# Kernel optimization log

Measured on AMD Instinct MI355X. Metric: run time of the kernel, lower is better.

## Reference

```python
import jax, jax.numpy as jnp
import numpy as np

N_NODES = 50000
N_EDGES = 800000
F_IN = 128
F_OUT = 64


def setup_inputs() -> dict:
    key = jax.random.key(0)
    k_x, k_w, k_r, k_c, k_v = jax.random.split(key, 5)
    x = jax.random.normal(k_x, (N_NODES, F_IN), dtype=jnp.float32)
    weight = jax.random.normal(k_w, (F_IN, F_OUT), dtype=jnp.float32)
    edge_row = jnp.sort(jax.random.randint(k_r, (N_EDGES,), 0, N_NODES, dtype=jnp.int32))
    edge_col = jax.random.randint(k_c, (N_EDGES,), 0, N_NODES, dtype=jnp.int32)
    edge_val = jax.random.uniform(k_v, (N_EDGES,), dtype=jnp.float32)
    return {"x": x, "weight": weight, "edge_row": edge_row,
            "edge_col": edge_col, "edge_val": edge_val}


def reference(x, weight, edge_row, edge_col, edge_val):
    # pre_sup = dot(x, W)                      : [N, F_out] dense GEMM
    pre_sup = x @ weight
    # support @ pre_sup (sparse-dense matmul) via COO gather + segment sum:
    # out[r] = sum_{e: row[e]==r} val[e] * pre_sup[col[e]]
    msgs = edge_val[:, None] * pre_sup[edge_col]          # [E, F_out]
    out = jax.ops.segment_sum(msgs, edge_row, num_segments=N_NODES)
    # act = relu, no bias
    return jax.nn.relu(out)
```

## Files before the change

kernel.cpp:

```cpp
#include <hip/hip_runtime.h>
#include <hip/hip_bf16.h>

#define F_IN 128
#define F_OUT 64

typedef __attribute__((ext_vector_type(8))) short short8;
typedef __attribute__((ext_vector_type(4))) float f32x4;

__device__ __forceinline__ unsigned short f2bf_rne(float f) {
  unsigned int u = __builtin_bit_cast(unsigned int, f);
  u += 0x7fffu + ((u >> 16) & 1u);
  return (unsigned short)(u >> 16);
}
__device__ __forceinline__ float bfu2f(unsigned short u) {
  return __builtin_bit_cast(float, (unsigned int)u << 16);
}

__global__ __launch_bounds__(256) void gcn_gemm_rowptr(
    const float* __restrict__ x, const float* __restrict__ w,
    unsigned short* __restrict__ pre,
    const int* __restrict__ edge_row, int* __restrict__ row_ptr,
    int n_nodes, int n_edges, int gemm_blocks) {
  const int tid = threadIdx.x;

  if (blockIdx.x >= gemm_blocks) {
    const int r = (blockIdx.x - gemm_blocks) * 256 + tid;
    if (r > n_nodes) return;
    int lo = 0, hi = n_edges;
    while (lo < hi) {
      const int mid = (lo + hi) >> 1;
      if (edge_row[mid] < r) lo = mid + 1; else hi = mid;
    }
    row_ptr[r] = lo;
    return;
  }

  __shared__ __align__(16) unsigned short wt_hi[64 * 128];

  {
#pragma unroll
    for (int i = 0; i < 8; ++i) {
      const int flat4 = tid + i * 256;
      const float4 v = ((const float4*)w)[flat4];
      const float fv[4] = {v.x, v.y, v.z, v.w};
#pragma unroll
      for (int j = 0; j < 4; ++j) {
        const int flat = flat4 * 4 + j;
        const int k = flat >> 6;
        const int n = flat & 63;
        int off = (n << 8) + (k << 1);
        off ^= (n & 7) << 4;
        *(unsigned short*)((char*)wt_hi + off) = f2bf_rne(fv[j]);
      }
    }
  }
  __syncthreads();

  const int lane = tid & 63;
  const int mt = blockIdx.x * 4 + (tid >> 6);
  const int m0 = mt * 16;
  if (m0 >= n_nodes) return;

  const int lrow = lane & 15;
  const int lk = lane >> 4;
  const bool full = (m0 + 16 <= n_nodes);
  const int arow = full ? (m0 + lrow) : min(m0 + lrow, n_nodes - 1);

  f32x4 acc[4];
#pragma unroll
  for (int i = 0; i < 4; ++i) acc[i] = (f32x4){0.f, 0.f, 0.f, 0.f};

#pragma unroll
  for (int ks = 0; ks < 4; ++ks) {
    const float4* xp =
        (const float4*)(x + (size_t)arow * F_IN + ks * 32 + lk * 8);
    const float4 q0 = xp[0];
    const float4 q1 = xp[1];
    const float fv[8] = {q0.x, q0.y, q0.z, q0.w, q1.x, q1.y, q1.z, q1.w};
    short8 ah, al;
#pragma unroll
    for (int i = 0; i < 8; ++i) {
      const unsigned short h = f2bf_rne(fv[i]);
      ah[i] = (short)h;
      al[i] = (short)f2bf_rne(fv[i] - bfu2f(h));
    }
#pragma unroll
    for (int nt = 0; nt < 4; ++nt) {
      const int n = nt * 16 + lrow;
      int off = (n << 8) + (ks * 64 + lk * 16);
      off ^= (n & 7) << 4;
      const short8 bh = *(const short8*)((const char*)wt_hi + off);
      acc[nt] = __builtin_amdgcn_mfma_f32_16x16x32_bf16(ah, bh, acc[nt], 0, 0, 0);
      acc[nt] = __builtin_amdgcn_mfma_f32_16x16x32_bf16(al, bh, acc[nt], 0, 0, 0);
    }
  }

#pragma unroll
  for (int nt = 0; nt < 4; ++nt) {
#pragma unroll
    for (int r = 0; r < 4; ++r) {
      const int row = m0 + lk * 4 + r;
      if (full || row < n_nodes)
        pre[(size_t)row * F_OUT + nt * 16 + lrow] = f2bf_rne(acc[nt][r]);
    }
  }
}

__global__ __launch_bounds__(256) void gcn_spmm(
    const unsigned short* __restrict__ pre, const int* __restrict__ row_ptr,
    const int* __restrict__ edge_col, const float* __restrict__ edge_val,
    float* __restrict__ out, int n_nodes) {
  const int lane = threadIdx.x & 63;
  const int half = lane >> 5;
  const int fl = lane & 31;
  int row = (int)((blockIdx.x * blockDim.x + threadIdx.x) >> 6);
  row = __builtin_amdgcn_readfirstlane(row);
  if (row >= n_nodes) return;
  const int e0 = row_ptr[row];
  const int e1 = row_ptr[row + 1];

  float a0 = 0.f, a1 = 0.f, a2 = 0.f, a3 = 0.f;

  for (int base = e0; base < e1; base += 64) {
    const int cnt = min(64, e1 - base);
    int myc = 0;
    float myv = 0.f;
    if (lane < cnt) {
      myc = edge_col[base + lane] << 6;
      myv = edge_val[base + lane];
    }
    const int nb = (cnt + 15) >> 4;
    for (int b = 0; b < nb; ++b) {
      const int j0 = b * 16;
#pragma unroll
      for (int u = 0; u < 8; u += 2) {
        const int i0 = j0 + u * 2 + half;
        const int i1 = j0 + (u + 1) * 2 + half;
        const int c0 = __shfl(myc, i0);
        const float v0 = __shfl(myv, i0);
        const int c1 = __shfl(myc, i1);
        const float v1 = __shfl(myv, i1);
        const unsigned int p0 =
            *(const unsigned int*)((const char*)pre + ((size_t)c0 << 1) + (fl << 2));
        const unsigned int p1 =
            *(const unsigned int*)((const char*)pre + ((size_t)c1 << 1) + (fl << 2));
        a0 = fmaf(v0, bfu2f((unsigned short)(p0 & 0xffff)), a0);
        a1 = fmaf(v0, bfu2f((unsigned short)(p0 >> 16)), a1);
        a2 = fmaf(v1, bfu2f((unsigned short)(p1 & 0xffff)), a2);
        a3 = fmaf(v1, bfu2f((unsigned short)(p1 >> 16)), a3);
      }
    }
  }

  float s0 = (a0 + a2) + __shfl_xor(a0 + a2, 32);
  float s1 = (a1 + a3) + __shfl_xor(a1 + a3, 32);
  if (half == 0) {
    float2 o = make_float2(fmaxf(s0, 0.f), fmaxf(s1, 0.f));
    *(float2*)(out + (size_t)row * F_OUT + fl * 2) = o;
  }
}

extern "C" void kernel_launch(void* const* d_in, const int* in_sizes, int n_in,
                              void* d_out, int out_size, void* d_ws, size_t ws_size,
                              hipStream_t stream) {
  const float* x        = (const float*)d_in[0];
  const float* w        = (const float*)d_in[1];
  const int*   edge_row = (const int*)d_in[2];
  const int*   edge_col = (const int*)d_in[3];
  const float* edge_val = (const float*)d_in[4];
  float* out = (float*)d_out;

  const int n_nodes = in_sizes[0] / F_IN;
  const int n_edges = in_sizes[2];

  unsigned short* pre = (unsigned short*)d_ws;
  int* row_ptr = (int*)((char*)d_ws +
                        (size_t)n_nodes * F_OUT * sizeof(unsigned short));

  const int m_tiles = (n_nodes + 15) / 16;
  const int gemm_blocks = (m_tiles + 3) / 4;
  const int rp_blocks = (n_nodes + 1 + 255) / 256;
  gcn_gemm_rowptr<<<gemm_blocks + rp_blocks, 256, 0, stream>>>(
      x, w, pre, edge_row, row_ptr, n_nodes, n_edges, gemm_blocks);

  const int spmm_blocks = ((size_t)n_nodes * 64 + 255) / 256;
  gcn_spmm<<<spmm_blocks, 256, 0, stream>>>(pre, row_ptr, edge_col, edge_val,
                                            out, n_nodes);
}
```

Baseline: 32.65 us.

## Split SpMM wave into four edge groups with 8-byte gathers

Restructures the SpMM so each wavefront processes four edges at once, with 16 lanes per edge each loading 4 bf16 features (uint2) instead of two edges with 32 lanes loading 2 features. Edge indices and values are read directly with uniform scalar loads instead of being staged into lanes and broadcast via shuffles, and a tail loop handles leftovers. Partial sums are reduced with two xor-shuffle stages before a float4 write of the relu'd output. This is meant to cut shuffle overhead and widen the gather loads, at the cost of a deeper cross-lane reduction and more per-iteration scalar loads.

```diff
diff --git a/kernel.cpp b/kernel.cpp
--- a/kernel.cpp
+++ b/kernel.cpp
@@ -14,6 +14,12 @@
 }
 __device__ __forceinline__ float bfu2f(unsigned short u) {
   return __builtin_bit_cast(float, (unsigned int)u << 16);
+}
+__device__ __forceinline__ float bf_lo(unsigned int u) {
+  return __builtin_bit_cast(float, u << 16);
+}
+__device__ __forceinline__ float bf_hi(unsigned int u) {
+  return __builtin_bit_cast(float, u & 0xffff0000u);
 }
 
 __global__ __launch_bounds__(256) void gcn_gemm_rowptr(
@@ -111,8 +117,8 @@
     const int* __restrict__ edge_col, const float* __restrict__ edge_val,
     float* __restrict__ out, int n_nodes) {
   const int lane = threadIdx.x & 63;
-  const int half = lane >> 5;
-  const int fl = lane & 31;
+  const int q  = lane >> 4;
+  const int fl = lane & 15;
   int row = (int)((blockIdx.x * blockDim.x + threadIdx.x) >> 6);
   row = __builtin_amdgcn_readfirstlane(row);
   if (row >= n_nodes) return;
@@ -120,43 +126,56 @@
   const int e1 = row_ptr[row + 1];
 
   float a0 = 0.f, a1 = 0.f, a2 = 0.f, a3 = 0.f;
-
-  for (int base = e0; base < e1; base += 64) {
-    const int cnt = min(64, e1 - base);
-    int myc = 0;
-    float myv = 0.f;
-    if (lane < cnt) {
-      myc = edge_col[base + lane] << 6;
-      myv = edge_val[base + lane];
-    }
-    const int nb = (cnt + 15) >> 4;
-    for (int b = 0; b < nb; ++b) {
-      const int j0 = b * 16;
-#pragma unroll
-      for (int u = 0; u < 8; u += 2) {
-        const int i0 = j0 + u * 2 + half;
-        const int i1 = j0 + (u + 1) * 2 + half;
-        const int c0 = __shfl(myc, i0);
-        const float v0 = __shfl(myv, i0);
-        const int c1 = __shfl(myc, i1);
-        const float v1 = __shfl(myv, i1);
-        const unsigned int p0 =
-            *(const unsigned int*)((const char*)pre + ((size_t)c0 << 1) + (fl << 2));
-        const unsigned int p1 =
-            *(const unsigned int*)((const char*)pre + ((size_t)c1 << 1) + (fl << 2));
-        a0 = fmaf(v0, bfu2f((unsigned short)(p0 & 0xffff)), a0);
-        a1 = fmaf(v0, bfu2f((unsigned short)(p0 >> 16)), a1);
-        a2 = fmaf(v1, bfu2f((unsigned short)(p1 & 0xffff)), a2);
-        a3 = fmaf(v1, bfu2f((unsigned short)(p1 >> 16)), a3);
-      }
-    }
-  }
-
-  float s0 = (a0 + a2) + __shfl_xor(a0 + a2, 32);
-  float s1 = (a1 + a3) + __shfl_xor(a1 + a3, 32);
-  if (half == 0) {
-    float2 o = make_float2(fmaxf(s0, 0.f), fmaxf(s1, 0.f));
-    *(float2*)(out + (size_t)row * F_OUT + fl * 2) = o;
+  const char* prebase = (const char*)pre + ((size_t)fl << 3);
+
+  int e = e0;
+  for (; e + 16 <= e1; e += 16) {
+#pragma unroll
+    for (int g = 0; g < 4; ++g) {
+      const int   cA = edge_col[e + g * 4 + 0];
+      const int   cB = edge_col[e + g * 4 + 1];
+      const int   cC = edge_col[e + g * 4 + 2];
+      const int   cD = edge_col[e + g * 4 + 3];
+      const float vA = edge_val[e + g * 4 + 0];
+      const float vB = edge_val[e + g * 4 + 1];
+      const float vC = edge_val[e + g * 4 + 2];
+      const float vD = edge_val[e + g * 4 + 3];
+      const int   cc = q < 2 ? (q == 0 ? cA : cB) : (q == 2 ? cC : cD);
+      const float vv = q < 2 ? (q == 0 ? vA : vB) : (q == 2 ? vC : vD);
+      const uint2 p = *(const uint2*)(prebase + ((size_t)cc << 7));
+      a0 = fmaf(vv, bf_lo(p.x), a0);
+      a1 = fmaf(vv, bf_hi(p.x), a1);
+      a2 = fmaf(vv, bf_lo(p.y), a2);
+      a3 = fmaf(vv, bf_hi(p.y), a3);
+    }
+  }
+  for (; e < e1; e += 4) {
+    const int idx = e + q;
+    int cc = 0;
+    float vv = 0.f;
+    if (idx < e1) {
+      cc = edge_col[idx];
+      vv = edge_val[idx];
+    }
+    const uint2 p = *(const uint2*)(prebase + ((size_t)cc << 7));
+    a0 = fmaf(vv, bf_lo(p.x), a0);
+    a1 = fmaf(vv, bf_hi(p.x), a1);
+    a2 = fmaf(vv, bf_lo(p.y), a2);
+    a3 = fmaf(vv, bf_hi(p.y), a3);
+  }
+
+  a0 += __shfl_xor(a0, 16); a0 += __shfl_xor(a0, 32);
+  a1 += __shfl_xor(a1, 16); a1 += __shfl_xor(a1, 32);
+  a2 += __shfl_xor(a2, 16); a2 += __shfl_xor(a2, 32);
+  a3 += __shfl_xor(a3, 16); a3 += __shfl_xor(a3, 32);
+
+  if (q == 0) {
+    float4 o;
+    o.x = fmaxf(a0, 0.f);
+    o.y = fmaxf(a1, 0.f);
+    o.z = fmaxf(a2, 0.f);
+    o.w = fmaxf(a3, 0.f);
+    *(float4*)(out + (size_t)row * F_OUT + fl * 4) = o;
   }
 }
 
```

New measurement: 38.84 us. 1.19x slower.
